# Optimization experiments

Measured on AMD Instinct MI355X. Metric: run time of the kernel, lower is better.

The kernel has to match this reference:

```python
import jax, jax.numpy as jnp
import numpy as np

N_NODES = 50000
N_EDGES = 800000
D_FEAT = 128
HIDDEN = 128
N_GRAPHS = 64


def setup_inputs() -> dict:
    key = jax.random.key(0)
    ks = jax.random.split(key, 16)
    x = jax.random.normal(ks[0], (N_NODES, D_FEAT), dtype=jnp.float32)
    edge_index = jax.random.randint(ks[1], (2, N_EDGES), 0, N_NODES, dtype=jnp.int64)
    batch = jnp.sort(jax.random.randint(ks[2], (N_NODES,), 0, N_GRAPHS, dtype=jnp.int64))

    def lin(k, fan_in, fan_out):
        kw, kb = jax.random.split(k)
        bound = 1.0 / np.sqrt(fan_in)
        W = jax.random.uniform(kw, (fan_in, fan_out), minval=-bound, maxval=bound, dtype=jnp.float32)
        b = jax.random.uniform(kb, (fan_out,), minval=-bound, maxval=bound, dtype=jnp.float32)
        return W, b

    W1, b1 = lin(ks[3], D_FEAT, HIDDEN)
    W2, b2 = lin(ks[4], HIDDEN, HIDDEN)
    W3, b3 = lin(ks[5], HIDDEN, HIDDEN)
    fw1, fb1 = lin(ks[6], HIDDEN, 64)
    fw2, fb2 = lin(ks[7], 64, 32)
    fw3, fb3 = lin(ks[8], 32, 1)
    return {"x": x, "W1": W1, "b1": b1, "W2": W2, "b2": b2, "W3": W3, "b3": b3,
            "fw1": fw1, "fb1": fb1, "fw2": fw2, "fb2": fb2, "fw3": fw3, "fb3": fb3,
            "edge_index": edge_index, "batch": batch}


def _gcn_norm(edge_index, n_nodes):
    # add self-loops, compute symmetric degree normalization (PyG GCNConv default)
    loop = jnp.arange(n_nodes, dtype=edge_index.dtype)
    src = jnp.concatenate([edge_index[0], loop])  # [E+N]
    dst = jnp.concatenate([edge_index[1], loop])
    deg = jax.ops.segment_sum(jnp.ones_like(dst, dtype=jnp.float32), dst, num_segments=n_nodes)
    dinv = jnp.where(deg > 0, jax.lax.rsqrt(jnp.maximum(deg, 1.0)), 0.0)
    norm = dinv[src] * dinv[dst]  # [E+N]
    return src, dst, norm


def _gcn_conv(x, W, b, src, dst, norm, n_nodes):
    h = x @ W                                   # [N, out]
    msg = h[src] * norm[:, None]                # gather over edges
    out = jax.ops.segment_sum(msg, dst, num_segments=n_nodes)  # scatter-add
    return out + b


def reference(x, W1, b1, W2, b2, W3, b3, fw1, fb1, fw2, fb2, fw3, fb3, edge_index, batch):
    n = x.shape[0]
    src, dst, norm = _gcn_norm(edge_index, n)
    h = jax.nn.elu(_gcn_conv(x, W1, b1, src, dst, norm, n))
    h = jax.nn.elu(_gcn_conv(h, W2, b2, src, dst, norm, n))
    h = _gcn_conv(h, W3, b3, src, dst, norm, n)
    # global mean pool over graphs
    sums = jax.ops.segment_sum(h, batch, num_segments=N_GRAPHS)        # [G, H]
    cnt = jax.ops.segment_sum(jnp.ones((n,), jnp.float32), batch, num_segments=N_GRAPHS)
    g = sums / jnp.maximum(cnt, 1.0)[:, None]
    g = jax.nn.relu(g @ fw1 + fb1)
    g = jax.nn.relu(g @ fw2 + fb2)
    return g @ fw3 + fb3  # [G, 1]
```

## Files before the change

### kernel.cpp

```cpp
#include <hip/hip_runtime.h>

#define D 128
#define NG 64

#define SCAN_CHUNK 16
#define SCAN_BLOCK 256
#define SCAN_TILE (SCAN_CHUNK * SCAN_BLOCK)

#define FILL_CHUNKS 128

typedef unsigned short ushort_t;
typedef unsigned int uint_t;
typedef __attribute__((ext_vector_type(8))) short short8;
typedef __attribute__((ext_vector_type(4))) float f32x4;

__device__ __forceinline__ float bflo(uint_t w) { return __uint_as_float(w << 16); }
__device__ __forceinline__ float bfhi(uint_t w) { return __uint_as_float(w & 0xFFFF0000u); }
__device__ __forceinline__ float bf2f(ushort_t u) { return __uint_as_float(((uint_t)u) << 16); }
__device__ __forceinline__ ushort_t f2bf(float f) {
  uint_t x = __float_as_uint(f);
  x = x + 0x7FFFu + ((x >> 16) & 1u);
  return (ushort_t)(x >> 16);
}

static constexpr int OW1 = 0, OB1 = 16384, OW2 = 16512, OB2 = 32896, OW3 = 33024,
                     OB3 = 49408, OFW1 = 49536, OFB1 = 57728, OFW2 = 57792,
                     OFB2 = 59840, OFW3 = 59872, OFB3 = 59904, WTOT = 59905;

__global__ void detect_kernel(const ushort_t* __restrict__ x, int* __restrict__ flag) {
  __shared__ int bad;
  if (threadIdx.x == 0) bad = 0;
  __syncthreads();
  int b = 0;
  for (int i = threadIdx.x; i < 4096; i += 256) {
    ushort_t u = x[i];
    int e = (u >> 7) & 0xFF;
    float v = bf2f(u);
    if (e == 0xFF || fabsf(v) > 1e6f) b++;
  }
  if (b) atomicAdd(&bad, b);
  __syncthreads();
  if (threadIdx.x == 0) *flag = (bad == 0) ? 1 : 0;
}

__global__ __launch_bounds__(256) void convert_params(
    const void* W1, const void* b1, const void* W2, const void* b2,
    const void* W3, const void* b3, const void* fw1, const void* fb1,
    const void* fw2, const void* fb2, const void* fw3, const void* fb3,
    const int* __restrict__ flag, float* __restrict__ out) {
  int i = blockIdx.x * 256 + threadIdx.x;
  if (i >= WTOT) return;
  const void* src; int local;
  if      (i < OB1)  { src = W1;  local = i; }
  else if (i < OW2)  { src = b1;  local = i - OB1; }
  else if (i < OB2)  { src = W2;  local = i - OW2; }
  else if (i < OW3)  { src = b2;  local = i - OB2; }
  else if (i < OB3)  { src = W3;  local = i - OW3; }
  else if (i < OFW1) { src = b3;  local = i - OB3; }
  else if (i < OFB1) { src = fw1; local = i - OFW1; }
  else if (i < OFW2) { src = fb1; local = i - OFB1; }
  else if (i < OFB2) { src = fw2; local = i - OFW2; }
  else if (i < OFW3) { src = fb2; local = i - OFB2; }
  else if (i < OFB3) { src = fw3; local = i - OFW3; }
  else               { src = fb3; local = i - OFB3; }
  bool bf = (*flag != 0);
  out[i] = bf ? bf2f(((const ushort_t*)src)[local]) : ((const float*)src)[local];
}

__global__ __launch_bounds__(256) void wtrans_kernel(const float* __restrict__ wconv,
                                                     ushort_t* __restrict__ wt) {
  int i = blockIdx.x * 256 + threadIdx.x;
  if (i >= 3 * 16384) return;
  int L = i >> 14, rem = i & 16383;
  int nIdx = rem >> 7, k = rem & 127;
  int base = (L == 0) ? OW1 : (L == 1) ? OW2 : OW3;
  wt[i] = f2bf(wconv[base + k * D + nIdx]);
}

__global__ __launch_bounds__(256) void deg_kernel(const int* __restrict__ ei,
                                                  int* __restrict__ deg, int E, int octSize) {
  const int oct = blockIdx.x & 7;
  const int chunkSz = (E + FILL_CHUNKS - 1) / FILL_CHUNKS;
  const int c0 = (blockIdx.x >> 3) * chunkSz;
  const int c1 = min(c0 + chunkSz, E);
  const int lo = oct * octSize, hi = lo + octSize;
  for (int i = c0 + threadIdx.x; i < c1; i += 256) {
    int dst = __builtin_nontemporal_load(&ei[E + i]);
    if (dst >= lo && dst < hi) atomicAdd(&deg[dst], 1);
  }
}

__global__ void dinv_kernel(const int* __restrict__ deg, float* __restrict__ dinv, int n) {
  int i = blockIdx.x * 256 + threadIdx.x;
  if (i < n) dinv[i] = rsqrtf((float)(deg[i] + 1));
}

__global__ __launch_bounds__(SCAN_BLOCK) void scan_phase1(const int* __restrict__ deg,
                                                          int* __restrict__ blockSum, int n) {
  __shared__ int sh[SCAN_BLOCK];
  const int t = threadIdx.x;
  const int base = blockIdx.x * SCAN_TILE + t * SCAN_CHUNK;
  int s = 0;
  #pragma unroll
  for (int i = 0; i < SCAN_CHUNK; i++) {
    int idx = base + i;
    if (idx < n) s += deg[idx];
  }
  sh[t] = s;
  __syncthreads();
  for (int off = SCAN_BLOCK / 2; off > 0; off >>= 1) {
    if (t < off) sh[t] += sh[t + off];
    __syncthreads();
  }
  if (t == 0) blockSum[blockIdx.x] = sh[0];
}

__global__ void scan_phase2(int* __restrict__ blockSum, int* __restrict__ row, int nb, int n) {
  int acc = 0;
  for (int i = 0; i < nb; i++) { int v = blockSum[i]; blockSum[i] = acc; acc += v; }
  row[n] = acc;
}

__global__ __launch_bounds__(SCAN_BLOCK) void scan_phase3(const int* __restrict__ deg,
                                                          const int* __restrict__ blockSum,
                                                          int* __restrict__ row,
                                                          int* __restrict__ cur, int n) {
  __shared__ int sh[SCAN_BLOCK];
  const int t = threadIdx.x;
  const int base = blockIdx.x * SCAN_TILE + t * SCAN_CHUNK;
  int v[SCAN_CHUNK];
  int s = 0;
  #pragma unroll
  for (int i = 0; i < SCAN_CHUNK; i++) {
    int idx = base + i;
    v[i] = (idx < n) ? deg[idx] : 0;
    s += v[i];
  }
  sh[t] = s;
  __syncthreads();
  for (int off = 1; off < SCAN_BLOCK; off <<= 1) {
    int val = (t >= off) ? sh[t - off] : 0;
    __syncthreads();
    sh[t] += val;
    __syncthreads();
  }
  int excl = ((t == 0) ? 0 : sh[t - 1]) + blockSum[blockIdx.x];
  #pragma unroll
  for (int i = 0; i < SCAN_CHUNK; i++) {
    int idx = base + i;
    if (idx < n) { row[idx] = excl; cur[idx] = excl; excl += v[i]; }
  }
}

__global__ __launch_bounds__(256) void fill_kernel(const int* __restrict__ ei,
                                                   int* __restrict__ cur,
                                                   int* __restrict__ csr, int E, int octSize) {
  const int oct = blockIdx.x & 7;
  const int chunkSz = (E + FILL_CHUNKS - 1) / FILL_CHUNKS;
  const int c0 = (blockIdx.x >> 3) * chunkSz;
  const int c1 = min(c0 + chunkSz, E);
  const int lo = oct * octSize, hi = lo + octSize;
  for (int i = c0 + threadIdx.x; i < c1; i += 256) {
    int dst = __builtin_nontemporal_load(&ei[E + i]);
    if (dst >= lo && dst < hi) {
      int src = __builtin_nontemporal_load(&ei[i]);
      int pos = atomicAdd(&cur[dst], 1);
      csr[pos] = src;
    }
  }
}

__global__ __launch_bounds__(256) void gemm128_mfma(const void* __restrict__ Ain,
                                                    const ushort_t* __restrict__ Wt,
                                                    const float* __restrict__ dinv,
                                                    ushort_t* __restrict__ out, int n,
                                                    const int* __restrict__ flag,
                                                    int src_is_input) {
  __shared__ ushort_t wlds[128 * 128];
  const int tid = threadIdx.x;

  {
    const uint4* srcp = (const uint4*)Wt;
    uint4* dstp = (uint4*)wlds;
    #pragma unroll
    for (int i = 0; i < 8; i++) {
      int c = tid + i * 256;
      dstp[c ^ ((c >> 4) & 7)] = srcp[c];
    }
  }
  __syncthreads();

  const int w = tid >> 6, lane = tid & 63;
  const int lrow = lane & 15, lk = lane >> 4;
  const int r0 = blockIdx.x * 64 + w * 16;
  const int node = r0 + lrow;
  const bool bf = src_is_input ? (*flag != 0) : true;

  f32x4 acc[8];
  #pragma unroll
  for (int t = 0; t < 8; t++) acc[t] = (f32x4){0.f, 0.f, 0.f, 0.f};

  #pragma unroll
  for (int ks = 0; ks < 4; ks++) {
    short8 af;
    if (node < n) {
      if (bf) {
        af = *reinterpret_cast<const short8*>(
            (const ushort_t*)Ain + (size_t)node * D + ks * 32 + lk * 8);
      } else {
        const float* Af = (const float*)Ain + (size_t)node * D + ks * 32 + lk * 8;
        float4 a0 = *reinterpret_cast<const float4*>(Af);
        float4 a1 = *reinterpret_cast<const float4*>(Af + 4);
        af = (short8){(short)f2bf(a0.x), (short)f2bf(a0.y), (short)f2bf(a0.z), (short)f2bf(a0.w),
                      (short)f2bf(a1.x), (short)f2bf(a1.y), (short)f2bf(a1.z), (short)f2bf(a1.w)};
      }
    } else {
      af = (short8){0, 0, 0, 0, 0, 0, 0, 0};
    }
    #pragma unroll
    for (int t = 0; t < 8; t++) {
      int chunk = (t * 16 + lrow) * 16 + ks * 4 + lk;
      int swz = chunk ^ (lrow & 7);
      short8 bfrag = *reinterpret_cast<const short8*>((const uint4*)wlds + swz);
      acc[t] = __builtin_amdgcn_mfma_f32_16x16x32_bf16(af, bfrag, acc[t], 0, 0, 0);
    }
  }

  __syncthreads();

  float dv[4];
  #pragma unroll
  for (int j = 0; j < 4; j++) {
    int r = r0 + lk * 4 + j;
    dv[j] = (r < n) ? dinv[r] : 0.f;
  }
  ushort_t* st = wlds + w * 16 * D;
  #pragma unroll
  for (int t = 0; t < 8; t++) {
    #pragma unroll
    for (int j = 0; j < 4; j++) {
      int rr = lk * 4 + j;
      int idx = rr * D + t * 16 + lrow;
      st[idx ^ ((rr & 7) << 3)] = f2bf(acc[t][j] * dv[j]);
    }
  }
  __syncthreads();

  const int rrow = lane >> 2;
  const int cbase = (lane & 3) * 8;
  #pragma unroll
  for (int it = 0; it < 4; it++) {
    int col = cbase + it * 32;
    int idx = rrow * D + col;
    uint4 v = *reinterpret_cast<const uint4*>(&st[idx ^ ((rrow & 7) << 3)]);
    if (r0 + rrow < n)
      *reinterpret_cast<uint4*>(&out[(size_t)(r0 + rrow) * D + col]) = v;
  }
}

__global__ __launch_bounds__(256) void aggregate(const ushort_t* __restrict__ h,
                                                 const int* __restrict__ row,
                                                 const int* __restrict__ csr,
                                                 const float* __restrict__ dinv,
                                                 const float* __restrict__ bias,
                                                 ushort_t* __restrict__ out, int n, int do_elu) {
  const int gid = (blockIdx.x * 256 + threadIdx.x) >> 6;
  const int lane = threadIdx.x & 63;
  if (gid >= n) return;
  uint_t hv = *reinterpret_cast<const uint_t*>(&h[(size_t)gid * D + lane * 2]);
  float ax = bflo(hv), ay = bfhi(hv);
  const int s = row[gid], e = row[gid + 1];
  int idx = s;
  for (; idx + 7 < e; idx += 8) {
    int s0 = csr[idx],     s1 = csr[idx + 1], s2 = csr[idx + 2], s3 = csr[idx + 3];
    int s4 = csr[idx + 4], s5 = csr[idx + 5], s6 = csr[idx + 6], s7 = csr[idx + 7];
    uint_t m0 = *reinterpret_cast<const uint_t*>(&h[(size_t)s0 * D + lane * 2]);
    uint_t m1 = *reinterpret_cast<const uint_t*>(&h[(size_t)s1 * D + lane * 2]);
    uint_t m2 = *reinterpret_cast<const uint_t*>(&h[(size_t)s2 * D + lane * 2]);
    uint_t m3 = *reinterpret_cast<const uint_t*>(&h[(size_t)s3 * D + lane * 2]);
    uint_t m4 = *reinterpret_cast<const uint_t*>(&h[(size_t)s4 * D + lane * 2]);
    uint_t m5 = *reinterpret_cast<const uint_t*>(&h[(size_t)s5 * D + lane * 2]);
    uint_t m6 = *reinterpret_cast<const uint_t*>(&h[(size_t)s6 * D + lane * 2]);
    uint_t m7 = *reinterpret_cast<const uint_t*>(&h[(size_t)s7 * D + lane * 2]);
    ax += bflo(m0); ay += bfhi(m0);
    ax += bflo(m1); ay += bfhi(m1);
    ax += bflo(m2); ay += bfhi(m2);
    ax += bflo(m3); ay += bfhi(m3);
    ax += bflo(m4); ay += bfhi(m4);
    ax += bflo(m5); ay += bfhi(m5);
    ax += bflo(m6); ay += bfhi(m6);
    ax += bflo(m7); ay += bfhi(m7);
  }
  for (; idx + 3 < e; idx += 4) {
    int s0 = csr[idx], s1 = csr[idx + 1], s2 = csr[idx + 2], s3 = csr[idx + 3];
    uint_t m0 = *reinterpret_cast<const uint_t*>(&h[(size_t)s0 * D + lane * 2]);
    uint_t m1 = *reinterpret_cast<const uint_t*>(&h[(size_t)s1 * D + lane * 2]);
    uint_t m2 = *reinterpret_cast<const uint_t*>(&h[(size_t)s2 * D + lane * 2]);
    uint_t m3 = *reinterpret_cast<const uint_t*>(&h[(size_t)s3 * D + lane * 2]);
    ax += bflo(m0); ay += bfhi(m0);
    ax += bflo(m1); ay += bfhi(m1);
    ax += bflo(m2); ay += bfhi(m2);
    ax += bflo(m3); ay += bfhi(m3);
  }
  for (; idx < e; idx++) {
    int s0 = csr[idx];
    uint_t m0 = *reinterpret_cast<const uint_t*>(&h[(size_t)s0 * D + lane * 2]);
    ax += bflo(m0); ay += bfhi(m0);
  }
  const float di = dinv[gid];
  float2 bv = *reinterpret_cast<const float2*>(&bias[lane * 2]);
  float ox = ax * di + bv.x;
  float oy = ay * di + bv.y;
  if (do_elu) {
    ox = ox > 0.f ? ox : expm1f(ox);
    oy = oy > 0.f ? oy : expm1f(oy);
  }
  uint_t o = (uint_t)f2bf(ox) | ((uint_t)f2bf(oy) << 16);
  *reinterpret_cast<uint_t*>(&out[(size_t)gid * D + lane * 2]) = o;
}

__global__ __launch_bounds__(256) void pool_kernel(const ushort_t* __restrict__ h,
                                                   const int* __restrict__ batch,
                                                   float* __restrict__ pooled, int n) {
  const int c  = threadIdx.x & 63;
  const int rl = threadIdx.x >> 6;
  const int base = blockIdx.x * 64;
  if (base >= n) return;
  const int end = min(base + 64, n);
  float sx = 0.f, sy = 0.f;
  int curg = -1;
  for (int i = base + rl; i < end; i += 4) {
    int g = batch[i];
    if (g != curg) {
      if (curg >= 0) {
        unsafeAtomicAdd(&pooled[curg * D + 2 * c], sx);
        unsafeAtomicAdd(&pooled[curg * D + 2 * c + 1], sy);
      }
      curg = g; sx = 0.f; sy = 0.f;
    }
    uint_t v = *reinterpret_cast<const uint_t*>(&h[(size_t)i * D + 2 * c]);
    sx += bflo(v); sy += bfhi(v);
  }
  if (curg >= 0) {
    unsafeAtomicAdd(&pooled[curg * D + 2 * c], sx);
    unsafeAtomicAdd(&pooled[curg * D + 2 * c + 1], sy);
  }
}

__global__ void cnt_kernel(const int* __restrict__ batch, float* __restrict__ cnt, int n) {
  int g = threadIdx.x;
  int lo = 0, hi = n;
  while (lo < hi) { int mid = (lo + hi) >> 1; if (batch[mid] < g) lo = mid + 1; else hi = mid; }
  int a = lo;
  lo = 0; hi = n;
  while (lo < hi) { int mid = (lo + hi) >> 1; if (batch[mid] < g + 1) lo = mid + 1; else hi = mid; }
  cnt[g] = (float)(lo - a);
}

__global__ __launch_bounds__(64) void mlp_kernel(const float* __restrict__ pooled,
                                                 const float* __restrict__ cnt,
                                                 const float* __restrict__ wf,
                                                 float* __restrict__ out) {
  __shared__ float g[128], h1[64], h2[32];
  const int gi = blockIdx.x, t = threadIdx.x;
  float c = fmaxf(cnt[gi], 1.0f);
  g[t] = pooled[gi * D + t] / c;
  g[t + 64] = pooled[gi * D + 64 + t] / c;
  __syncthreads();
  float a = wf[OFB1 + t];
  for (int k = 0; k < 128; k++) a += g[k] * wf[OFW1 + k * 64 + t];
  h1[t] = fmaxf(a, 0.f);
  __syncthreads();
  if (t < 32) {
    float a2 = wf[OFB2 + t];
    for (int k = 0; k < 64; k++) a2 += h1[k] * wf[OFW2 + k * 32 + t];
    h2[t] = fmaxf(a2, 0.f);
  }
  __syncthreads();
  if (t == 0) {
    float a3 = wf[OFB3];
    for (int k = 0; k < 32; k++) a3 += h2[k] * wf[OFW3 + k];
    out[gi] = a3;
  }
}

extern "C" void kernel_launch(void* const* d_in, const int* in_sizes, int n_in,
                              void* d_out, int out_size, void* d_ws, size_t ws_size,
                              hipStream_t stream) {
  (void)n_in; (void)out_size; (void)ws_size;
  const int* ei    = (const int*)d_in[13];
  const int* batch = (const int*)d_in[14];
  const int N = in_sizes[14];
  const int E = in_sizes[13] / 2;
  const int octSize = (N + 7) / 8;

  char* ws = (char*)d_ws;
  size_t off = 0;
  auto take = [&](size_t bytes) -> char* {
    char* p = ws + off;
    off += (bytes + 255) & ~(size_t)255;
    return p;
  };
  int*     flag   = (int*)take(4);
  int*     deg    = (int*)take((size_t)N * 4);
  float*   dinv   = (float*)take((size_t)N * 4);
  int*     row    = (int*)take((size_t)(N + 1) * 4);
  int*     cur    = (int*)take((size_t)N * 4);
  int*     csr    = (int*)take((size_t)E * 4);
  float*   wconv  = (float*)take((size_t)WTOT * 4);
  ushort_t* wt    = (ushort_t*)take((size_t)3 * 16384 * 2);
  int*     bsum   = (int*)take(1024 * 4);
  ushort_t* bufA  = (ushort_t*)take((size_t)N * D * 2);
  ushort_t* bufB  = (ushort_t*)take((size_t)N * D * 2);
  float*   pooled = (float*)take((size_t)NG * D * 4);
  float*   cnt    = (float*)take((size_t)NG * 4);

  hipMemsetAsync(deg, 0, (size_t)N * 4, stream);
  hipMemsetAsync(pooled, 0, (size_t)NG * D * 4, stream);

  detect_kernel<<<1, 256, 0, stream>>>((const ushort_t*)d_in[0], flag);
  convert_params<<<(WTOT + 255) / 256, 256, 0, stream>>>(
      d_in[1], d_in[2], d_in[3], d_in[4], d_in[5], d_in[6], d_in[7], d_in[8],
      d_in[9], d_in[10], d_in[11], d_in[12], flag, wconv);
  wtrans_kernel<<<192, 256, 0, stream>>>(wconv, wt);

  deg_kernel<<<FILL_CHUNKS * 8, 256, 0, stream>>>(ei, deg, E, octSize);
  dinv_kernel<<<(N + 255) / 256, 256, 0, stream>>>(deg, dinv, N);

  const int nbScan = (N + SCAN_TILE - 1) / SCAN_TILE;
  scan_phase1<<<nbScan, SCAN_BLOCK, 0, stream>>>(deg, bsum, N);
  scan_phase2<<<1, 1, 0, stream>>>(bsum, row, nbScan, N);
  scan_phase3<<<nbScan, SCAN_BLOCK, 0, stream>>>(deg, bsum, row, cur, N);

  fill_kernel<<<FILL_CHUNKS * 8, 256, 0, stream>>>(ei, cur, csr, E, octSize);

  const int gemm_grid = (N + 63) / 64;
  const int agg_grid = (N * 64 + 255) / 256;

  gemm128_mfma<<<gemm_grid, 256, 0, stream>>>(d_in[0], wt, dinv, bufA, N, flag, 1);
  aggregate<<<agg_grid, 256, 0, stream>>>(bufA, row, csr, dinv, wconv + OB1, bufB, N, 1);
  gemm128_mfma<<<gemm_grid, 256, 0, stream>>>((const void*)bufB, wt + 16384, dinv, bufA, N, flag, 0);
  aggregate<<<agg_grid, 256, 0, stream>>>(bufA, row, csr, dinv, wconv + OB2, bufB, N, 1);
  gemm128_mfma<<<gemm_grid, 256, 0, stream>>>((const void*)bufB, wt + 32768, dinv, bufA, N, flag, 0);
  aggregate<<<agg_grid, 256, 0, stream>>>(bufA, row, csr, dinv, wconv + OB3, bufB, N, 0);

  pool_kernel<<<(N + 63) / 64, 256, 0, stream>>>(bufB, batch, pooled, N);
  cnt_kernel<<<1, NG, 0, stream>>>(batch, cnt, N);
  mlp_kernel<<<NG, 64, 0, stream>>>(pooled, cnt, wconv, (float*)d_out);
}
```

Measured before the change: 276.3 us.

## Merge setup kernels, vectorize edge loads, and grid-stride aggregation

Combines the dtype-detect, parameter-convert and weight-transpose kernels into one launch. It folds dinv into scan phase 1 and drops the serial scan phase 2 by having each phase-3 block sum the earlier block totals. It also moves the count computation into the pool kernel. The degree and CSR-fill kernels now read edge indices as 4-wide vectors, and aggregation switches to a fixed 2048-block grid-stride loop. The goal is fewer launches and serial steps, at the cost of redundant prefix sums per block and possible load imbalance in aggregation.

```diff
diff --git a/kernel.cpp b/kernel.cpp
--- a/kernel.cpp
+++ b/kernel.cpp
@@ -7,12 +7,13 @@
 #define SCAN_BLOCK 256
 #define SCAN_TILE (SCAN_CHUNK * SCAN_BLOCK)
 
-#define FILL_CHUNKS 128
+#define FILL_CHUNKS 125
 
 typedef unsigned short ushort_t;
 typedef unsigned int uint_t;
 typedef __attribute__((ext_vector_type(8))) short short8;
 typedef __attribute__((ext_vector_type(4))) float f32x4;
+typedef __attribute__((ext_vector_type(4))) int i32x4;
 
 __device__ __forceinline__ float bflo(uint_t w) { return __uint_as_float(w << 16); }
 __device__ __forceinline__ float bfhi(uint_t w) { return __uint_as_float(w & 0xFFFF0000u); }
@@ -26,8 +27,14 @@
 static constexpr int OW1 = 0, OB1 = 16384, OW2 = 16512, OB2 = 32896, OW3 = 33024,
                      OB3 = 49408, OFW1 = 49536, OFB1 = 57728, OFW2 = 57792,
                      OFB2 = 59840, OFW3 = 59872, OFB3 = 59904, WTOT = 59905;
-
-__global__ void detect_kernel(const ushort_t* __restrict__ x, int* __restrict__ flag) {
+static constexpr int WT_ELEMS = 3 * 16384;
+
+__global__ __launch_bounds__(256) void params_kernel(
+    const ushort_t* __restrict__ x,
+    const void* W1, const void* b1, const void* W2, const void* b2,
+    const void* W3, const void* b3, const void* fw1, const void* fb1,
+    const void* fw2, const void* fb2, const void* fw3, const void* fb3,
+    int* __restrict__ flag, float* __restrict__ wconv, ushort_t* __restrict__ wt) {
   __shared__ int bad;
   if (threadIdx.x == 0) bad = 0;
   __syncthreads();
@@ -35,67 +42,67 @@
   for (int i = threadIdx.x; i < 4096; i += 256) {
     ushort_t u = x[i];
     int e = (u >> 7) & 0xFF;
-    float v = bf2f(u);
-    if (e == 0xFF || fabsf(v) > 1e6f) b++;
+    if (e == 0xFF || fabsf(bf2f(u)) > 1e6f) b++;
   }
   if (b) atomicAdd(&bad, b);
   __syncthreads();
-  if (threadIdx.x == 0) *flag = (bad == 0) ? 1 : 0;
-}
-
-__global__ __launch_bounds__(256) void convert_params(
-    const void* W1, const void* b1, const void* W2, const void* b2,
-    const void* W3, const void* b3, const void* fw1, const void* fb1,
-    const void* fw2, const void* fb2, const void* fw3, const void* fb3,
-    const int* __restrict__ flag, float* __restrict__ out) {
+  const bool bf = (bad == 0);
+  if (blockIdx.x == 0 && threadIdx.x == 0) *flag = bf ? 1 : 0;
+
   int i = blockIdx.x * 256 + threadIdx.x;
-  if (i >= WTOT) return;
-  const void* src; int local;
-  if      (i < OB1)  { src = W1;  local = i; }
-  else if (i < OW2)  { src = b1;  local = i - OB1; }
-  else if (i < OB2)  { src = W2;  local = i - OW2; }
-  else if (i < OW3)  { src = b2;  local = i - OB2; }
-  else if (i < OB3)  { src = W3;  local = i - OW3; }
-  else if (i < OFW1) { src = b3;  local = i - OB3; }
-  else if (i < OFB1) { src = fw1; local = i - OFW1; }
-  else if (i < OFW2) { src = fb1; local = i - OFB1; }
-  else if (i < OFB2) { src = fw2; local = i - OFW2; }
-  else if (i < OFW3) { src = fb2; local = i - OFB2; }
-  else if (i < OFB3) { src = fw3; local = i - OFW3; }
-  else               { src = fb3; local = i - OFB3; }
-  bool bf = (*flag != 0);
-  out[i] = bf ? bf2f(((const ushort_t*)src)[local]) : ((const float*)src)[local];
-}
-
-__global__ __launch_bounds__(256) void wtrans_kernel(const float* __restrict__ wconv,
-                                                     ushort_t* __restrict__ wt) {
-  int i = blockIdx.x * 256 + threadIdx.x;
-  if (i >= 3 * 16384) return;
-  int L = i >> 14, rem = i & 16383;
-  int nIdx = rem >> 7, k = rem & 127;
-  int base = (L == 0) ? OW1 : (L == 1) ? OW2 : OW3;
-  wt[i] = f2bf(wconv[base + k * D + nIdx]);
+  if (i < WTOT) {
+    const void* src; int local;
+    if      (i < OB1)  { src = W1;  local = i; }
+    else if (i < OW2)  { src = b1;  local = i - OB1; }
+    else if (i < OB2)  { src = W2;  local = i - OW2; }
+    else if (i < OW3)  { src = b2;  local = i - OB2; }
+    else if (i < OB3)  { src = W3;  local = i - OW3; }
+    else if (i < OFW1) { src = b3;  local = i - OB3; }
+    else if (i < OFB1) { src = fw1; local = i - OFW1; }
+    else if (i < OFW2) { src = fb1; local = i - OFB1; }
+    else if (i < OFB2) { src = fw2; local = i - OFW2; }
+    else if (i < OFW3) { src = fb2; local = i - OFB2; }
+    else if (i < OFB3) { src = fw3; local = i - OFW3; }
+    else               { src = fb3; local = i - OFB3; }
+    wconv[i] = bf ? bf2f(((const ushort_t*)src)[local]) : ((const float*)src)[local];
+  } else if (i < WTOT + WT_ELEMS) {
+    int j = i - WTOT;
+    int L = j >> 14, rem = j & 16383;
+    int nIdx = rem >> 7, k = rem & 127;
+    const void* src = (L == 0) ? W1 : (L == 1) ? W2 : W3;
+    int idx = k * D + nIdx;
+    float v = bf ? bf2f(((const ushort_t*)src)[idx]) : ((const float*)src)[idx];
+    wt[j] = f2bf(v);
+  }
 }
 
 __global__ __launch_bounds__(256) void deg_kernel(const int* __restrict__ ei,
                                                   int* __restrict__ deg, int E, int octSize) {
   const int oct = blockIdx.x & 7;
-  const int chunkSz = (E + FILL_CHUNKS - 1) / FILL_CHUNKS;
+  int chunkSz = ((E + FILL_CHUNKS - 1) / FILL_CHUNKS + 3) & ~3;
   const int c0 = (blockIdx.x >> 3) * chunkSz;
   const int c1 = min(c0 + chunkSz, E);
   const int lo = oct * octSize, hi = lo + octSize;
-  for (int i = c0 + threadIdx.x; i < c1; i += 256) {
-    int dst = __builtin_nontemporal_load(&ei[E + i]);
-    if (dst >= lo && dst < hi) atomicAdd(&deg[dst], 1);
-  }
-}
-
-__global__ void dinv_kernel(const int* __restrict__ deg, float* __restrict__ dinv, int n) {
-  int i = blockIdx.x * 256 + threadIdx.x;
-  if (i < n) dinv[i] = rsqrtf((float)(deg[i] + 1));
+  if ((E & 3) == 0) {
+    const int ng = (c1 - c0) >> 2;
+    for (int g = threadIdx.x; g < ng; g += 256) {
+      i32x4 d = __builtin_nontemporal_load(
+          reinterpret_cast<const i32x4*>(&ei[E + c0 + g * 4]));
+      if (d.x >= lo && d.x < hi) atomicAdd(&deg[d.x], 1);
+      if (d.y >= lo && d.y < hi) atomicAdd(&deg[d.y], 1);
+      if (d.z >= lo && d.z < hi) atomicAdd(&deg[d.z], 1);
+      if (d.w >= lo && d.w < hi) atomicAdd(&deg[d.w], 1);
+    }
+  } else {
+    for (int i = c0 + threadIdx.x; i < c1; i += 256) {
+      int dst = __builtin_nontemporal_load(&ei[E + i]);
+      if (dst >= lo && dst < hi) atomicAdd(&deg[dst], 1);
+    }
+  }
 }
 
 __global__ __launch_bounds__(SCAN_BLOCK) void scan_phase1(const int* __restrict__ deg,
+                                                          float* __restrict__ dinv,
                                                           int* __restrict__ blockSum, int n) {
   __shared__ int sh[SCAN_BLOCK];
   const int t = threadIdx.x;
@@ -104,7 +111,11 @@
   #pragma unroll
   for (int i = 0; i < SCAN_CHUNK; i++) {
     int idx = base + i;
-    if (idx < n) s += deg[idx];
+    if (idx < n) {
+      int dg = deg[idx];
+      s += dg;
+      dinv[idx] = rsqrtf((float)(dg + 1));
+    }
   }
   sh[t] = s;
   __syncthreads();
@@ -115,19 +126,15 @@
   if (t == 0) blockSum[blockIdx.x] = sh[0];
 }
 
-__global__ void scan_phase2(int* __restrict__ blockSum, int* __restrict__ row, int nb, int n) {
-  int acc = 0;
-  for (int i = 0; i < nb; i++) { int v = blockSum[i]; blockSum[i] = acc; acc += v; }
-  row[n] = acc;
-}
-
 __global__ __launch_bounds__(SCAN_BLOCK) void scan_phase3(const int* __restrict__ deg,
                                                           const int* __restrict__ blockSum,
                                                           int* __restrict__ row,
-                                                          int* __restrict__ cur, int n) {
+                                                          int* __restrict__ cur, int n, int nb) {
   __shared__ int sh[SCAN_BLOCK];
   const int t = threadIdx.x;
   const int base = blockIdx.x * SCAN_TILE + t * SCAN_CHUNK;
+  int pre = 0;
+  for (int bm = 0; bm < (int)blockIdx.x; bm++) pre += blockSum[bm];
   int v[SCAN_CHUNK];
   int s = 0;
   #pragma unroll
@@ -144,28 +151,45 @@
     sh[t] += val;
     __syncthreads();
   }
-  int excl = ((t == 0) ? 0 : sh[t - 1]) + blockSum[blockIdx.x];
+  int excl = ((t == 0) ? 0 : sh[t - 1]) + pre;
   #pragma unroll
   for (int i = 0; i < SCAN_CHUNK; i++) {
     int idx = base + i;
     if (idx < n) { row[idx] = excl; cur[idx] = excl; excl += v[i]; }
   }
+  if ((int)blockIdx.x == nb - 1 && t == SCAN_BLOCK - 1) row[n] = pre + sh[SCAN_BLOCK - 1];
 }
 
 __global__ __launch_bounds__(256) void fill_kernel(const int* __restrict__ ei,
                                                    int* __restrict__ cur,
                                                    int* __restrict__ csr, int E, int octSize) {
   const int oct = blockIdx.x & 7;
-  const int chunkSz = (E + FILL_CHUNKS - 1) / FILL_CHUNKS;
+  int chunkSz = ((E + FILL_CHUNKS - 1) / FILL_CHUNKS + 3) & ~3;
   const int c0 = (blockIdx.x >> 3) * chunkSz;
   const int c1 = min(c0 + chunkSz, E);
   const int lo = oct * octSize, hi = lo + octSize;
-  for (int i = c0 + threadIdx.x; i < c1; i += 256) {
-    int dst = __builtin_nontemporal_load(&ei[E + i]);
-    if (dst >= lo && dst < hi) {
-      int src = __builtin_nontemporal_load(&ei[i]);
-      int pos = atomicAdd(&cur[dst], 1);
-      csr[pos] = src;
+  if ((E & 3) == 0) {
+    const int ng = (c1 - c0) >> 2;
+    for (int g = threadIdx.x; g < ng; g += 256) {
+      const int base = c0 + g * 4;
+      i32x4 d = __builtin_nontemporal_load(reinterpret_cast<const i32x4*>(&ei[E + base]));
+      bool h0 = d.x >= lo && d.x < hi, h1 = d.y >= lo && d.y < hi;
+      bool h2 = d.z >= lo && d.z < hi, h3 = d.w >= lo && d.w < hi;
+      if (h0 | h1 | h2 | h3) {
+        i32x4 sv = __builtin_nontemporal_load(reinterpret_cast<const i32x4*>(&ei[base]));
+        if (h0) csr[atomicAdd(&cur[d.x], 1)] = sv.x;
+        if (h1) csr[atomicAdd(&cur[d.y], 1)] = sv.y;
+        if (h2) csr[atomicAdd(&cur[d.z], 1)] = sv.z;
+        if (h3) csr[atomicAdd(&cur[d.w], 1)] = sv.w;
+      }
+    }
+  } else {
+    for (int i = c0 + threadIdx.x; i < c1; i += 256) {
+      int dst = __builtin_nontemporal_load(&ei[E + i]);
+      if (dst >= lo && dst < hi) {
+        int src = __builtin_nontemporal_load(&ei[i]);
+        csr[atomicAdd(&cur[dst], 1)] = src;
+      }
     }
   }
 }
@@ -264,64 +288,76 @@
                                                  const float* __restrict__ dinv,
                                                  const float* __restrict__ bias,
                                                  ushort_t* __restrict__ out, int n, int do_elu) {
-  const int gid = (blockIdx.x * 256 + threadIdx.x) >> 6;
+  const int wid = (blockIdx.x * 256 + threadIdx.x) >> 6;
+  const int nw = (gridDim.x * 256) >> 6;
   const int lane = threadIdx.x & 63;
-  if (gid >= n) return;
-  uint_t hv = *reinterpret_cast<const uint_t*>(&h[(size_t)gid * D + lane * 2]);
-  float ax = bflo(hv), ay = bfhi(hv);
-  const int s = row[gid], e = row[gid + 1];
-  int idx = s;
-  for (; idx + 7 < e; idx += 8) {
-    int s0 = csr[idx],     s1 = csr[idx + 1], s2 = csr[idx + 2], s3 = csr[idx + 3];
-    int s4 = csr[idx + 4], s5 = csr[idx + 5], s6 = csr[idx + 6], s7 = csr[idx + 7];
-    uint_t m0 = *reinterpret_cast<const uint_t*>(&h[(size_t)s0 * D + lane * 2]);
-    uint_t m1 = *reinterpret_cast<const uint_t*>(&h[(size_t)s1 * D + lane * 2]);
-    uint_t m2 = *reinterpret_cast<const uint_t*>(&h[(size_t)s2 * D + lane * 2]);
-    uint_t m3 = *reinterpret_cast<const uint_t*>(&h[(size_t)s3 * D + lane * 2]);
-    uint_t m4 = *reinterpret_cast<const uint_t*>(&h[(size_t)s4 * D + lane * 2]);
-    uint_t m5 = *reinterpret_cast<const uint_t*>(&h[(size_t)s5 * D + lane * 2]);
-    uint_t m6 = *reinterpret_cast<const uint_t*>(&h[(size_t)s6 * D + lane * 2]);
-    uint_t m7 = *reinterpret_cast<const uint_t*>(&h[(size_t)s7 * D + lane * 2]);
-    ax += bflo(m0); ay += bfhi(m0);
-    ax += bflo(m1); ay += bfhi(m1);
-    ax += bflo(m2); ay += bfhi(m2);
-    ax += bflo(m3); ay += bfhi(m3);
-    ax += bflo(m4); ay += bfhi(m4);
-    ax += bflo(m5); ay += bfhi(m5);
-    ax += bflo(m6); ay += bfhi(m6);
-    ax += bflo(m7); ay += bfhi(m7);
-  }
-  for (; idx + 3 < e; idx += 4) {
-    int s0 = csr[idx], s1 = csr[idx + 1], s2 = csr[idx + 2], s3 = csr[idx + 3];
-    uint_t m0 = *reinterpret_cast<const uint_t*>(&h[(size_t)s0 * D + lane * 2]);
-    uint_t m1 = *reinterpret_cast<const uint_t*>(&h[(size_t)s1 * D + lane * 2]);
-    uint_t m2 = *reinterpret_cast<const uint_t*>(&h[(size_t)s2 * D + lane * 2]);
-    uint_t m3 = *reinterpret_cast<const uint_t*>(&h[(size_t)s3 * D + lane * 2]);
-    ax += bflo(m0); ay += bfhi(m0);
-    ax += bflo(m1); ay += bfhi(m1);
-    ax += bflo(m2); ay += bfhi(m2);
-    ax += bflo(m3); ay += bfhi(m3);
-  }
-  for (; idx < e; idx++) {
-    int s0 = csr[idx];
-    uint_t m0 = *reinterpret_cast<const uint_t*>(&h[(size_t)s0 * D + lane * 2]);
-    ax += bflo(m0); ay += bfhi(m0);
-  }
-  const float di = dinv[gid];
   float2 bv = *reinterpret_cast<const float2*>(&bias[lane * 2]);
-  float ox = ax * di + bv.x;
-  float oy = ay * di + bv.y;
-  if (do_elu) {
-    ox = ox > 0.f ? ox : expm1f(ox);
-    oy = oy > 0.f ? oy : expm1f(oy);
-  }
-  uint_t o = (uint_t)f2bf(ox) | ((uint_t)f2bf(oy) << 16);
-  *reinterpret_cast<uint_t*>(&out[(size_t)gid * D + lane * 2]) = o;
+  for (int gid = wid; gid < n; gid += nw) {
+    uint_t hv = *reinterpret_cast<const uint_t*>(&h[(size_t)gid * D + lane * 2]);
+    float ax = bflo(hv), ay = bfhi(hv);
+    const int s = row[gid], e = row[gid + 1];
+    int idx = s;
+    for (; idx + 7 < e; idx += 8) {
+      int s0 = csr[idx],     s1 = csr[idx + 1], s2 = csr[idx + 2], s3 = csr[idx + 3];
+      int s4 = csr[idx + 4], s5 = csr[idx + 5], s6 = csr[idx + 6], s7 = csr[idx + 7];
+      uint_t m0 = *reinterpret_cast<const uint_t*>(&h[(size_t)s0 * D + lane * 2]);
+      uint_t m1 = *reinterpret_cast<const uint_t*>(&h[(size_t)s1 * D + lane * 2]);
+      uint_t m2 = *reinterpret_cast<const uint_t*>(&h[(size_t)s2 * D + lane * 2]);
+      uint_t m3 = *reinterpret_cast<const uint_t*>(&h[(size_t)s3 * D + lane * 2]);
+      uint_t m4 = *reinterpret_cast<const uint_t*>(&h[(size_t)s4 * D + lane * 2]);
+      uint_t m5 = *reinterpret_cast<const uint_t*>(&h[(size_t)s5 * D + lane * 2]);
+      uint_t m6 = *reinterpret_cast<const uint_t*>(&h[(size_t)s6 * D + lane * 2]);
+      uint_t m7 = *reinterpret_cast<const uint_t*>(&h[(size_t)s7 * D + lane * 2]);
+      ax += bflo(m0); ay += bfhi(m0);
+      ax += bflo(m1); ay += bfhi(m1);
+      ax += bflo(m2); ay += bfhi(m2);
+      ax += bflo(m3); ay += bfhi(m3);
+      ax += bflo(m4); ay += bfhi(m4);
+      ax += bflo(m5); ay += bfhi(m5);
+      ax += bflo(m6); ay += bfhi(m6);
+      ax += bflo(m7); ay += bfhi(m7);
+    }
+    for (; idx + 3 < e; idx += 4) {
+      int s0 = csr[idx], s1 = csr[idx + 1], s2 = csr[idx + 2], s3 = csr[idx + 3];
+      uint_t m0 = *reinterpret_cast<const uint_t*>(&h[(size_t)s0 * D + lane * 2]);
+      uint_t m1 = *reinterpret_cast<const uint_t*>(&h[(size_t)s1 * D + lane * 2]);
+      uint_t m2 = *reinterpret_cast<const uint_t*>(&h[(size_t)s2 * D + lane * 2]);
+      uint_t m3 = *reinterpret_cast<const uint_t*>(&h[(size_t)s3 * D + lane * 2]);
+      ax += bflo(m0); ay += bfhi(m0);
+      ax += bflo(m1); ay += bfhi(m1);
+      ax += bflo(m2); ay += bfhi(m2);
+      ax += bflo(m3); ay += bfhi(m3);
+    }
+    for (; idx < e; idx++) {
+      int s0 = csr[idx];
+      uint_t m0 = *reinterpret_cast<const uint_t*>(&h[(size_t)s0 * D + lane * 2]);
+      ax += bflo(m0); ay += bfhi(m0);
+    }
+    const float di = dinv[gid];
+    float ox = ax * di + bv.x;
+    float oy = ay * di + bv.y;
+    if (do_elu) {
+      ox = ox > 0.f ? ox : expm1f(ox);
+      oy = oy > 0.f ? oy : expm1f(oy);
+    }
+    uint_t o = (uint_t)f2bf(ox) | ((uint_t)f2bf(oy) << 16);
+    *reinterpret_cast<uint_t*>(&out[(size_t)gid * D + lane * 2]) = o;
+  }
 }
 
 __global__ __launch_bounds__(256) void pool_kernel(const ushort_t* __restrict__ h,
                                                    const int* __restrict__ batch,
-                                                   float* __restrict__ pooled, int n) {
+                                                   float* __restrict__ pooled,
+                                                   float* __restrict__ cnt, int n) {
+  if (blockIdx.x == 0 && threadIdx.x < NG) {
+    int g = threadIdx.x;
+    int lo = 0, hi = n;
+    while (lo < hi) { int mid = (lo + hi) >> 1; if (batch[mid] < g) lo = mid + 1; else hi = mid; }
+    int a = lo;
+    lo = 0; hi = n;
+    while (lo < hi) { int mid = (lo + hi) >> 1; if (batch[mid] < g + 1) lo = mid + 1; else hi = mid; }
+    cnt[g] = (float)(lo - a);
+  }
   const int c  = threadIdx.x & 63;
   const int rl = threadIdx.x >> 6;
   const int base = blockIdx.x * 64;
@@ -347,16 +383,6 @@
   }
 }
 
-__global__ void cnt_kernel(const int* __restrict__ batch, float* __restrict__ cnt, int n) {
-  int g = threadIdx.x;
-  int lo = 0, hi = n;
-  while (lo < hi) { int mid = (lo + hi) >> 1; if (batch[mid] < g) lo = mid + 1; else hi = mid; }
-  int a = lo;
-  lo = 0; hi = n;
-  while (lo < hi) { int mid = (lo + hi) >> 1; if (batch[mid] < g + 1) lo = mid + 1; else hi = mid; }
-  cnt[g] = (float)(lo - a);
-}
-
 __global__ __launch_bounds__(64) void mlp_kernel(const float* __restrict__ pooled,
                                                  const float* __restrict__ cnt,
                                                  const float* __restrict__ wf,
@@ -408,7 +434,7 @@
   int*     cur    = (int*)take((size_t)N * 4);
   int*     csr    = (int*)take((size_t)E * 4);
   float*   wconv  = (float*)take((size_t)WTOT * 4);
-  ushort_t* wt    = (ushort_t*)take((size_t)3 * 16384 * 2);
+  ushort_t* wt    = (ushort_t*)take((size_t)WT_ELEMS * 2);
   int*     bsum   = (int*)take(1024 * 4);
   ushort_t* bufA  = (ushort_t*)take((size_t)N * D * 2);
   ushort_t* bufB  = (ushort_t*)take((size_t)N * D * 2);
@@ -418,24 +444,21 @@
   hipMemsetAsync(deg, 0, (size_t)N * 4, stream);
   hipMemsetAsync(pooled, 0, (size_t)NG * D * 4, stream);
 
-  detect_kernel<<<1, 256, 0, stream>>>((const ushort_t*)d_in[0], flag);
-  convert_params<<<(WTOT + 255) / 256, 256, 0, stream>>>(
-      d_in[1], d_in[2], d_in[3], d_in[4], d_in[5], d_in[6], d_in[7], d_in[8],
-      d_in[9], d_in[10], d_in[11], d_in[12], flag, wconv);
-  wtrans_kernel<<<192, 256, 0, stream>>>(wconv, wt);
+  const int pgrid = (WTOT + WT_ELEMS + 255) / 256;
+  params_kernel<<<pgrid, 256, 0, stream>>>(
+      (const ushort_t*)d_in[0], d_in[1], d_in[2], d_in[3], d_in[4], d_in[5], d_in[6],
+      d_in[7], d_in[8], d_in[9], d_in[10], d_in[11], d_in[12], flag, wconv, wt);
 
   deg_kernel<<<FILL_CHUNKS * 8, 256, 0, stream>>>(ei, deg, E, octSize);
-  dinv_kernel<<<(N + 255) / 256, 256, 0, stream>>>(deg, dinv, N);
 
   const int nbScan = (N + SCAN_TILE - 1) / SCAN_TILE;
-  scan_phase1<<<nbScan, SCAN_BLOCK, 0, stream>>>(deg, bsum, N);
-  scan_phase2<<<1, 1, 0, stream>>>(bsum, row, nbScan, N);
-  scan_phase3<<<nbScan, SCAN_BLOCK, 0, stream>>>(deg, bsum, row, cur, N);
+  scan_phase1<<<nbScan, SCAN_BLOCK, 0, stream>>>(deg, dinv, bsum, N);
+  scan_phase3<<<nbScan, SCAN_BLOCK, 0, stream>>>(deg, bsum, row, cur, N, nbScan);
 
   fill_kernel<<<FILL_CHUNKS * 8, 256, 0, stream>>>(ei, cur, csr, E, octSize);
 
   const int gemm_grid = (N + 63) / 64;
-  const int agg_grid = (N * 64 + 255) / 256;
+  const int agg_grid = 2048;
 
   gemm128_mfma<<<gemm_grid, 256, 0, stream>>>(d_in[0], wt, dinv, bufA, N, flag, 1);
   aggregate<<<agg_grid, 256, 0, stream>>>(bufA, row, csr, dinv, wconv + OB1, bufB, N, 1);
@@ -444,7 +467,6 @@
   gemm128_mfma<<<gemm_grid, 256, 0, stream>>>((const void*)bufB, wt + 32768, dinv, bufA, N, flag, 0);
   aggregate<<<agg_grid, 256, 0, stream>>>(bufA, row, csr, dinv, wconv + OB3, bufB, N, 0);
 
-  pool_kernel<<<(N + 63) / 64, 256, 0, stream>>>(bufB, batch, pooled, N);
-  cnt_kernel<<<1, NG, 0, stream>>>(batch, cnt, N);
+  pool_kernel<<<(N + 63) / 64, 256, 0, stream>>>(bufB, batch, pooled, cnt, N);
   mlp_kernel<<<NG, 64, 0, stream>>>(pooled, cnt, wconv, (float*)d_out);
 }
```

Result: faster. 265.1 us (-4.1%).
